# Kernel optimization log

Hardware: AMD Instinct MI355X
Metric: run time of the kernel (lower is better)

The kernel has to match this reference:

```python
import jax, jax.numpy as jnp
import numpy as np
from jax import lax

B, T, IDIM, HDIM = 128, 256, 64, 128
TS, KS, OC1, ANF = 64, 3, 100, 64
S1 = TS - 3 * (KS - 1)   # 58: three VALID ks=3 stride-1 convs
S = S1 * S1              # 3364
HN = 2 * HDIM            # 256 = h_dim * l_dim (l_dim=2)
F = S + HN               # 3620
HID = F // 2             # 1810


def _conv(x, w, b):
    y = lax.conv_general_dilated(x, w, (1, 1), 'VALID',
                                 dimension_numbers=('NCHW', 'OIHW', 'NCHW'))
    return y + b[None, :, None, None]


def _lstm_layer(x, w_ih, w_hh, b_ih, b_hh):
    # x: [B, T, D] -> (outputs [B, T, H], final hidden [B, H]); PyTorch gate order i,f,g,o
    Bn = x.shape[0]
    h0 = jnp.zeros((Bn, HDIM), x.dtype)
    c0 = jnp.zeros((Bn, HDIM), x.dtype)
    def step(carry, xt):
        h, c = carry
        g = xt @ w_ih.T + h @ w_hh.T + b_ih + b_hh
        i, f, gg, o = jnp.split(g, 4, axis=-1)
        c = jax.nn.sigmoid(f) * c + jax.nn.sigmoid(i) * jnp.tanh(gg)
        h = jax.nn.sigmoid(o) * jnp.tanh(c)
        return (h, c), h
    (hT, cT), ys = lax.scan(step, (h0, c0), jnp.swapaxes(x, 0, 1))
    return jnp.swapaxes(ys, 0, 1), hT


def setup_inputs() -> dict:
    key = jax.random.key(0)
    k = jax.random.split(key, 30)
    s = 0.05
    H4 = 4 * HDIM
    return {
        'x1': jax.random.normal(k[0], (B, 3, TS, TS), jnp.float32),
        'x2': jax.random.normal(k[1], (B, T, IDIM), jnp.float32),
        # conv2a/conv2b: two Monte-Carlo weight samples of the same Bayesian conv2 layer
        'conv1_w': jax.random.normal(k[2], (OC1, 3, KS, KS), jnp.float32) * s,
        'conv1_b': jax.random.normal(k[3], (OC1,), jnp.float32) * s,
        'conv2a_w': jax.random.normal(k[4], (OC1, OC1, KS, KS), jnp.float32) * s,
        'conv2a_b': jax.random.normal(k[5], (OC1,), jnp.float32) * s,
        'conv2b_w': jax.random.normal(k[6], (OC1, OC1, KS, KS), jnp.float32) * s,
        'conv2b_b': jax.random.normal(k[7], (OC1,), jnp.float32) * s,
        'w_ih0': jax.random.normal(k[8], (H4, IDIM), jnp.float32) * s,
        'w_hh0': jax.random.normal(k[9], (H4, HDIM), jnp.float32) * s,
        'b_ih0': jax.random.normal(k[10], (H4,), jnp.float32) * s,
        'b_hh0': jax.random.normal(k[11], (H4,), jnp.float32) * s,
        'w_ih1': jax.random.normal(k[12], (H4, HDIM), jnp.float32) * s,
        'w_hh1': jax.random.normal(k[13], (H4, HDIM), jnp.float32) * s,
        'b_ih1': jax.random.normal(k[14], (H4,), jnp.float32) * s,
        'b_hh1': jax.random.normal(k[15], (H4,), jnp.float32) * s,
        'attn1_w': jax.random.normal(k[16], (ANF, F), jnp.float32) * s,
        'attn1_b': jax.random.normal(k[17], (ANF,), jnp.float32) * s,
        'attn2_w': jax.random.normal(k[18], (1, ANF), jnp.float32) * s,
        'attn2_b': jax.random.normal(k[19], (1,), jnp.float32) * s,
        'fc1_w': jax.random.normal(k[20], (HID, F), jnp.float32) * s,
        'fc1_b': jax.random.normal(k[21], (HID,), jnp.float32) * s,
        'fc2_w': jax.random.normal(k[22], (1, HID), jnp.float32) * s,
        'fc2_b': jax.random.normal(k[23], (1,), jnp.float32) * s,
    }


def reference(x1, x2, conv1_w, conv1_b, conv2a_w, conv2a_b, conv2b_w, conv2b_b,
              w_ih0, w_hh0, b_ih0, b_hh0, w_ih1, w_hh1, b_ih1, b_hh1,
              attn1_w, attn1_b, attn2_w, attn2_b, fc1_w, fc1_b, fc2_w, fc2_b):
    Bn = x1.shape[0]
    # CNN branch
    x = jax.nn.relu(_conv(x1, conv1_w, conv1_b))
    x = jax.nn.relu(_conv(x, conv2a_w, conv2a_b))
    x = jax.nn.relu(_conv(x, conv2b_w, conv2b_b))
    xd = x.reshape(Bn, OC1, S)                               # [B, oc1, S]
    # LSTM branch (2 layers, dropout in eval mode = identity)
    y0, h0f = _lstm_layer(x2, w_ih0, w_hh0, b_ih0, b_hh0)
    _, h1f = _lstm_layer(y0, w_ih1, w_hh1, b_ih1, b_hh1)
    hn = jnp.concatenate([h0f, h1f], axis=1)                 # [B, 2*h_dim]
    # Broadcast hidden state across channels (replaces the torch concat loop)
    hn_b = jnp.broadcast_to(hn[:, None, :], (Bn, OC1, HN))
    fused = jnp.concatenate([xd, hn_b], axis=2)              # [B, oc1, F]
    # Attention
    a = jnp.tanh(fused @ attn1_w.T + attn1_b)                # [B, oc1, anf]
    a = a @ attn2_w.T + attn2_b                              # [B, oc1, 1]
    a = jax.nn.softmax(a, axis=1)
    ctx = jnp.einsum('bcs,bco->bso', xd, a).reshape(Bn, S)   # [B, S]
    # Fusion MLP (dropout eval-mode identity)
    m = jnp.concatenate([ctx, hn], axis=1)                   # [B, F]
    h = jax.nn.relu(m @ fc1_w.T + fc1_b)
    return h @ fc2_w.T + fc2_b                               # [B, 1]
```

## Files before the change

### kernel.cpp

```cpp
#include <hip/hip_runtime.h>
#include <hip/hip_bf16.h>
#include <math.h>

#define BB 128
#define TT 256
#define IDIM 64
#define HD 128
#define G4 512
#define OC 100
#define W1 62
#define W2 60
#define W3 58
#define NPX1 (W1*W1)
#define NPX2 (W2*W2)
#define NPX3 (W3*W3)
#define SS NPX3
#define FF (SS + 2*HD)
#define HIDN 1810
#define ANF 64

typedef __hip_bfloat16 bf16;
typedef _Float16 f16;
typedef __attribute__((ext_vector_type(8))) short bf16x8;
typedef __attribute__((ext_vector_type(4))) short bf16x4;
typedef __attribute__((ext_vector_type(2))) _Float16 half2v;
typedef __attribute__((ext_vector_type(4))) float f32x4;

__device__ __forceinline__ float ldf(const float* p) { return *p; }
__device__ __forceinline__ float ldf(const bf16* p)  { return __bfloat162float(*p); }
__device__ __forceinline__ void  stf(float* p, float v) { *p = v; }
__device__ __forceinline__ void  stf(bf16* p, float v)  { *p = __float2bfloat16(v); }

__device__ __forceinline__ short f2bs(float v) {
    bf16 t = __float2bfloat16(v); short s; __builtin_memcpy(&s, &t, 2); return s;
}
__device__ __forceinline__ float fsig(float x) {
    return __builtin_amdgcn_rcpf(1.f + __expf(-x));
}
__device__ __forceinline__ float ftanh(float x) {
    float t = __expf(-2.f * fabsf(x));
    float r = __builtin_amdgcn_rcpf(1.f + t);
    float m = 1.f - 2.f * t * r;
    return copysignf(m, x);
}
__device__ __forceinline__ float fmix2(unsigned w, unsigned h, float acc) {
    half2v wv, hv;
    __builtin_memcpy(&wv, &w, 4);
    __builtin_memcpy(&hv, &h, 4);
    acc = fmaf((float)wv[0], (float)hv[0], acc);
    acc = fmaf((float)wv[1], (float)hv[1], acc);
    return acc;
}

__device__ __forceinline__ bf16x8 load8(const bf16* p) { return *(const bf16x8*)p; }
__device__ __forceinline__ bf16x8 load8(const float* p) {
    float4 x = *(const float4*)p;
    float4 y = *(const float4*)(p + 4);
    bf16x8 r;
    r[0] = f2bs(x.x); r[1] = f2bs(x.y); r[2] = f2bs(x.z); r[3] = f2bs(x.w);
    r[4] = f2bs(y.x); r[5] = f2bs(y.y); r[6] = f2bs(y.z); r[7] = f2bs(y.w);
    return r;
}

__global__ void zero_kernel(float* o, int n)
{
    int i = blockIdx.x * 256 + threadIdx.x;
    if (i < n) o[i] = 0.f;
}

__global__ __launch_bounds__(256)
void cvt4_bf16(const float* __restrict__ s, bf16* __restrict__ d, int n4)
{
    int i = blockIdx.x * 256 + threadIdx.x;
    if (i >= n4) return;
    float4 v = ((const float4*)s)[i];
    bf16x4 o;
    o[0] = f2bs(v.x); o[1] = f2bs(v.y); o[2] = f2bs(v.z); o[3] = f2bs(v.w);
    *(bf16x4*)(d + 4 * (size_t)i) = o;
}

__global__ __launch_bounds__(256)
void cvt4_f16(const float* __restrict__ s, f16* __restrict__ d, int n4)
{
    int i = blockIdx.x * 256 + threadIdx.x;
    if (i >= n4) return;
    float4 v = ((const float4*)s)[i];
    f16 o[4] = {(f16)v.x, (f16)v.y, (f16)v.z, (f16)v.w};
    *(uint2*)(d + 4 * (size_t)i) = *(uint2*)o;
}

__global__ __launch_bounds__(256)
void conv1_kernel(const float* __restrict__ x1,
                  const float* __restrict__ w,
                  const float* __restrict__ bias,
                  bf16* __restrict__ out)
{
    __shared__ float wl[2700];
    __shared__ float bl[OC];
    int tid = threadIdx.x;
    for (int i = tid; i < 2700; i += 256) wl[i] = w[i];
    if (tid < OC) bl[tid] = bias[tid];
    __syncthreads();
    int b  = blockIdx.x;
    int px = blockIdx.y * 256 + tid;
    if (px >= NPX1) return;
    int y = px / W1, x = px % W1;
    float in[3][3][3];
    const float* xb = x1 + (size_t)b * 3 * 64 * 64;
#pragma unroll
    for (int ic = 0; ic < 3; ic++)
#pragma unroll
        for (int r = 0; r < 3; r++)
#pragma unroll
            for (int c = 0; c < 3; c++)
                in[ic][r][c] = xb[(ic * 64 + y + r) * 64 + x + c];
    bf16* ob = out + (size_t)b * OC * NPX1 + px;
    for (int oc = 0; oc < OC; ++oc) {
        float acc = bl[oc];
        const float* wp = &wl[oc * 27];
#pragma unroll
        for (int ic = 0; ic < 3; ic++)
#pragma unroll
            for (int r = 0; r < 3; r++)
#pragma unroll
                for (int c = 0; c < 3; c++)
                    acc = fmaf(in[ic][r][c], wp[ic * 9 + r * 3 + c], acc);
        ob[(size_t)oc * NPX1] = __float2bfloat16(fmaxf(acc, 0.f));
    }
}

__global__ __launch_bounds__(256)
void wt_repack(const float* __restrict__ w, bf16* __restrict__ WT)
{
    int idx = blockIdx.x * 256 + threadIdx.x;
    if (idx >= 129024) return;
    int i  = idx & 31;
    int oc = (idx >> 5) % 112;
    int ts = idx / (112 * 32);
    int s = ts & 3, t = ts >> 2;
    int ic = s * 32 + i;
    float v = 0.f;
    if (oc < OC && ic < OC) v = w[(oc * OC + ic) * 9 + t];
    WT[idx] = __float2bfloat16(v);
}

__global__ __launch_bounds__(512, 1)
void conv2_mfma(const bf16* __restrict__ in,
                const bf16* __restrict__ WT,
                const float* __restrict__ bias,
                bf16* __restrict__ out,
                int iw, int ow)
{
    __shared__ bf16 il[10 * 72 * 40];
    __shared__ bf16 wl[4032 * 8];
    int tid = threadIdx.x;
    int b = blockIdx.x;
    int y0 = blockIdx.y * 8;
    int wid = tid >> 6;
    int l = tid & 63;
    int hq = l >> 4;
    int l16 = l & 15;
    int yo = y0 + wid;

    f32x4 acc[7][4];
#pragma unroll
    for (int f = 0; f < 7; f++) {
#pragma unroll
        for (int r = 0; r < 4; r++) {
            int oc = f * 16 + hq * 4 + r;
            float bv = (oc < OC) ? bias[oc] : 0.f;
#pragma unroll
            for (int n = 0; n < 4; n++) acc[f][n][r] = bv;
        }
    }

    const size_t ims = (size_t)iw * iw;
    int icl = tid & 31;
    int t2  = tid >> 5;
    for (int s = 0; s < 4; ++s) {
        __syncthreads();
        int ic = s * 32 + icl;
        bool icok = ic < OC;
        const bf16* ibase = in + (size_t)(b * OC + ic) * ims;
#pragma unroll
        for (int it = 0; it < 6; ++it) {
            int u2 = t2 + it * 16;
            if (u2 < 90) {
                int r = u2 / 9, xb = u2 - r * 9;
                int x8 = xb * 8;
                int yy = y0 + r;
                bf16x8 v = {0, 0, 0, 0, 0, 0, 0, 0};
                if (icok && yy < iw && x8 < iw) {
                    const short* sp = (const short*)(ibase + (size_t)yy * iw + x8);
                    if (x8 + 8 <= iw) {
                        const unsigned* sp32 = (const unsigned*)sp;
#pragma unroll
                        for (int q = 0; q < 4; q++)
                            ((unsigned*)&v)[q] = sp32[q];
                    } else {
                        for (int k = 0; k < 8; k++)
                            if (x8 + k < iw) ((short*)&v)[k] = sp[k];
                    }
                }
                bf16* dst = &il[(r * 72 + x8) * 40 + icl];
#pragma unroll
                for (int k = 0; k < 8; k++)
                    *(short*)&dst[k * 40] = ((short*)&v)[k];
            }
        }
#pragma unroll
        for (int it = 0; it < 8; ++it) {
            int u = tid + it * 512;
            if (u < 4032) {
                int t = u / 448; int rem = u - t * 448;
                int oc = rem >> 2; int hq2 = rem & 3;
                *(bf16x8*)&wl[(size_t)((t * 4 + hq2) * 112 + oc) * 8] =
                    *(const bf16x8*)(WT + (size_t)((t * 4 + s) * 112 + oc) * 32 + hq2 * 8);
            }
        }
        __syncthreads();

#pragma unroll
        for (int ky = 0; ky < 3; ++ky) {
#pragma unroll
            for (int kx = 0; kx < 3; ++kx) {
                int t = ky * 3 + kx;
                bf16x8 a[7];
#pragma unroll
                for (int f = 0; f < 7; f++)
                    a[f] = *(const bf16x8*)&wl[(size_t)((t * 4 + hq) * 112 + f * 16 + l16) * 8];
                bf16x8 bfr[4];
#pragma unroll
                for (int n = 0; n < 4; n++)
                    bfr[n] = *(const bf16x8*)&il[((wid + ky) * 72 + kx + l16 + n * 16) * 40 + hq * 8];
#pragma unroll
                for (int f = 0; f < 7; f++)
#pragma unroll
                    for (int n = 0; n < 4; n++)
                        acc[f][n] = __builtin_amdgcn_mfma_f32_16x16x32_bf16(
                            a[f], bfr[n], acc[f][n], 0, 0, 0);
            }
        }
    }

    if (yo < ow) {
#pragma unroll
        for (int f = 0; f < 7; f++) {
#pragma unroll
            for (int r = 0; r < 4; r++) {
                int oc = f * 16 + hq * 4 + r;
                if (oc < OC) {
#pragma unroll
                    for (int n = 0; n < 4; n++) {
                        int x = n * 16 + l16;
                        if (x < ow)
                            out[((size_t)(b * OC + oc) * ow + yo) * ow + x] =
                                __float2bfloat16(fmaxf(acc[f][n][r], 0.f));
                    }
                }
            }
        }
    }
}

template<typename TB, typename TC, int ACT>
__global__ __launch_bounds__(256)
void gemm_mfma(const bf16* __restrict__ A, int lda,
               const TB* __restrict__ B, int ldb,
               const float* __restrict__ bias,
               TC* __restrict__ C, int ldc,
               int M, int N, int K)
{
    __shared__ bf16 As[64 * 72];
    __shared__ bf16 Bs[64 * 72];
    int tid = threadIdx.x;
    int l = tid & 63, wid = tid >> 6;
    int l16 = l & 15, h = l >> 4;
    int m0 = blockIdx.x * 64, n0 = blockIdx.y * 64;
    f32x4 acc[4];
#pragma unroll
    for (int nb = 0; nb < 4; nb++) acc[nb] = (f32x4){0.f, 0.f, 0.f, 0.f};

    int rs = tid >> 3;
    int kc = (tid & 7) * 8;

    for (int k0 = 0; k0 < K; k0 += 64) {
        int kr = K - k0;
#pragma unroll
        for (int half = 0; half < 2; half++) {
            int rr = rs + half * 32;
            bf16x8 av = {0, 0, 0, 0, 0, 0, 0, 0};
            int m = m0 + rr;
            if (m < M) {
                const short* src = (const short*)(A + (size_t)m * lda + k0 + kc);
                if (kc + 8 <= kr) av = *(const bf16x8*)src;
                else if (kc < kr) {
                    for (int j = 0; j < 8; j++) if (kc + j < kr) ((short*)&av)[j] = src[j];
                }
            }
            *(bf16x8*)&As[rr * 72 + kc] = av;
            bf16x8 bv = {0, 0, 0, 0, 0, 0, 0, 0};
            int n = n0 + rr;
            if (n < N) {
                const TB* src = B + (size_t)n * ldb + k0 + kc;
                if (kc + 8 <= kr) bv = load8(src);
                else if (kc < kr) {
                    for (int j = 0; j < 8; j++) if (kc + j < kr) ((short*)&bv)[j] = f2bs(ldf(src + j));
                }
            }
            *(bf16x8*)&Bs[rr * 72 + kc] = bv;
        }
        __syncthreads();
#pragma unroll
        for (int kk = 0; kk < 2; kk++) {
            bf16x8 af = *(const bf16x8*)&As[(wid * 16 + l16) * 72 + kk * 32 + h * 8];
#pragma unroll
            for (int nb = 0; nb < 4; nb++) {
                bf16x8 bfr = *(const bf16x8*)&Bs[(nb * 16 + l16) * 72 + kk * 32 + h * 8];
                acc[nb] = __builtin_amdgcn_mfma_f32_16x16x32_bf16(af, bfr, acc[nb], 0, 0, 0);
            }
        }
        __syncthreads();
    }
#pragma unroll
    for (int nb = 0; nb < 4; nb++) {
        int col = n0 + nb * 16 + l16;
        if (col >= N) continue;
        float bv = bias ? bias[col] : 0.f;
#pragma unroll
        for (int reg = 0; reg < 4; reg++) {
            int row = m0 + wid * 16 + h * 4 + reg;
            if (row < M) {
                float v = acc[nb][reg] + bv;
                if (ACT == 1) v = fmaxf(v, 0.f);
                stf(&C[(size_t)row * ldc + col], v);
            }
        }
    }
}

template<typename TA, typename TC, int BM, int BN, int BK, int TM, int TN, int ACT>
__global__ __launch_bounds__((BM / TM) * (BN / TN))
void gemm_tn(const TA* __restrict__ A, int lda,
             const float* __restrict__ Bmat, int ldb,
             const float* __restrict__ bias,
             TC* __restrict__ C, int ldc,
             int M, int N, int K)
{
    constexpr int TX = BN / TN;
    constexpr int TY = BM / TM;
    constexpr int NT = TX * TY;
    __shared__ float As[BK][BM + 1];
    __shared__ float Bs[BK][BN + 1];
    int tid = threadIdx.x;
    int tx = tid % TX, ty = tid / TX;
    int m0 = blockIdx.x * BM, n0 = blockIdx.y * BN;
    float acc[TM][TN] = {};
    for (int k0 = 0; k0 < K; k0 += BK) {
        for (int idx = tid; idx < BM * BK; idx += NT) {
            int i = idx / BK, j = idx % BK;
            int m = m0 + i, k = k0 + j;
            As[j][i] = (m < M && k < K) ? ldf(&A[(size_t)m * lda + k]) : 0.f;
        }
        for (int idx = tid; idx < BN * BK; idx += NT) {
            int i = idx / BK, j = idx % BK;
            int n = n0 + i, k = k0 + j;
            Bs[j][i] = (n < N && k < K) ? Bmat[(size_t)n * ldb + k] : 0.f;
        }
        __syncthreads();
#pragma unroll
        for (int k = 0; k < BK; ++k) {
            float av[TM], bv[TN];
#pragma unroll
            for (int i = 0; i < TM; i++) av[i] = As[k][ty * TM + i];
#pragma unroll
            for (int j = 0; j < TN; j++) bv[j] = Bs[k][tx * TN + j];
#pragma unroll
            for (int i = 0; i < TM; i++)
#pragma unroll
                for (int j = 0; j < TN; j++)
                    acc[i][j] += av[i] * bv[j];
        }
        __syncthreads();
    }
#pragma unroll
    for (int i = 0; i < TM; i++) {
        int m = m0 + ty * TM + i;
        if (m >= M) continue;
#pragma unroll
        for (int j = 0; j < TN; j++) {
            int n = n0 + tx * TN + j;
            if (n >= N) continue;
            float v = acc[i][j] + (bias ? bias[n] : 0.f);
            if (ACT == 1) v = fmaxf(v, 0.f);
            stf(&C[(size_t)m * ldc + n], v);
        }
    }
}

__global__ __launch_bounds__(512, 1)
void lstm_recur(const bf16* __restrict__ G,
                const f16* __restrict__ LWr,
                bf16* __restrict__ Y,
                float* __restrict__ HN,
                int hoff)
{
    __shared__ __align__(16) f16 hl[HD];
    __shared__ float ex[G4];
    int g = threadIdx.x;
    int b = blockIdx.x;
    uint4 wv[16];
    const uint4* wp = (const uint4*)(LWr + (size_t)g * HD);
#pragma unroll
    for (int q = 0; q < 16; q++) wv[q] = wp[q];
#pragma unroll
    for (int q = 0; q < 16; q++)
        asm volatile("" : "+v"(wv[q].x), "+v"(wv[q].y), "+v"(wv[q].z), "+v"(wv[q].w));
    float c = 0.f;
    if (g < HD) hl[g] = (f16)0.f;
    __syncthreads();
    const bf16* Gb = G + (size_t)b * TT * G4 + g;
    for (int t = 0; t < TT; ++t) {
        float dot = __bfloat162float(Gb[(size_t)t * G4]);
        float a0 = 0.f, a1 = 0.f, a2 = 0.f, a3 = 0.f;
#pragma unroll
        for (int q = 0; q < 16; q++) {
            uint4 hw = *(const uint4*)&hl[q * 8];
            a0 = fmix2(wv[q].x, hw.x, a0);
            a1 = fmix2(wv[q].y, hw.y, a1);
            a2 = fmix2(wv[q].z, hw.z, a2);
            a3 = fmix2(wv[q].w, hw.w, a3);
        }
        dot += (a0 + a1) + (a2 + a3);
        float tr;
        if (g < 2 * HD || g >= 3 * HD) tr = fsig(dot);
        else tr = ftanh(dot);
        ex[g] = tr;
        __syncthreads();
        if (g < HD) {
            float iv = ex[g], fv = ex[HD + g], gv = ex[2 * HD + g], ov = ex[3 * HD + g];
            c = fv * c + iv * gv;
            float nh = ov * ftanh(c);
            hl[g] = (f16)nh;
            if (Y) Y[((size_t)b * TT + t) * HD + g] = __float2bfloat16(nh);
            if (t == TT - 1) HN[(size_t)b * 256 + hoff + g] = nh;
        }
        __syncthreads();
    }
}

__global__ void bias_sum(const float* a, const float* b, float* o, int n)
{
    int i = blockIdx.x * 256 + threadIdx.x;
    if (i < n) o[i] = a[i] + b[i];
}

__global__ __launch_bounds__(128)
void attn_softmax(const float* __restrict__ T1,
                  const float* __restrict__ HB,
                  const float* __restrict__ a2w,
                  const float* __restrict__ a2b,
                  float* __restrict__ ATT)
{
    __shared__ float hbl[ANF];
    __shared__ float awl[ANF];
    __shared__ float red[128];
    int b = blockIdx.x, tid = threadIdx.x;
    if (tid < ANF) { hbl[tid] = HB[b * ANF + tid]; awl[tid] = a2w[tid]; }
    __syncthreads();
    float lg = -1e30f;
    if (tid < OC) {
        const float* tp = T1 + (size_t)(b * OC + tid) * ANF;
        float s = 0.f;
#pragma unroll 4
        for (int j = 0; j < ANF; j++) s += ftanh(tp[j] + hbl[j]) * awl[j];
        lg = s + a2b[0];
    }
    red[tid] = lg; __syncthreads();
    for (int st = 64; st > 0; st >>= 1) { if (tid < st) red[tid] = fmaxf(red[tid], red[tid + st]); __syncthreads(); }
    float mx = red[0]; __syncthreads();
    float e = (tid < OC) ? __expf(lg - mx) : 0.f;
    red[tid] = e; __syncthreads();
    for (int st = 64; st > 0; st >>= 1) { if (tid < st) red[tid] += red[tid + st]; __syncthreads(); }
    if (tid < OC) ATT[b * OC + tid] = e / red[0];
}

__global__ __launch_bounds__(256)
void ctx_concat(const bf16* __restrict__ XD,
                const float* __restrict__ ATT,
                const float* __restrict__ HN,
                bf16* __restrict__ M)
{
    __shared__ float al[OC];
    int b = blockIdx.x;
    int tid = threadIdx.x;
    if (tid < OC) al[tid] = ATT[b * OC + tid];
    __syncthreads();
    int s = blockIdx.y * 256 + tid;
    if (s < SS) {
        const bf16* xp = XD + (size_t)b * OC * SS + s;
        float acc = 0.f;
#pragma unroll 4
        for (int c = 0; c < OC; c++) acc = fmaf(__bfloat162float(xp[(size_t)c * SS]), al[c], acc);
        M[(size_t)b * FF + s] = __float2bfloat16(acc);
    } else if (s < FF) {
        M[(size_t)b * FF + s] = __float2bfloat16(HN[b * 256 + (s - SS)]);
    }
}

__global__ __launch_bounds__(256)
void fc2_kernel(const float* __restrict__ H1,
                const float* __restrict__ w,
                const float* __restrict__ bias,
                float* __restrict__ out)
{
    int tid = threadIdx.x;
    int lane = tid & 63, wid = tid >> 6;
    int b = blockIdx.x * 4 + wid;
    float acc = 0.f;
    for (int j = lane; j < HIDN; j += 64) acc = fmaf(H1[(size_t)b * HIDN + j], w[j], acc);
#pragma unroll
    for (int off = 32; off > 0; off >>= 1) acc += __shfl_down(acc, off, 64);
    if (lane == 0) out[b] = acc + bias[0];
}

extern "C" void kernel_launch(void* const* d_in, const int* in_sizes, int n_in,
                              void* d_out, int out_size, void* d_ws, size_t ws_size,
                              hipStream_t stream)
{
    const float* x1   = (const float*)d_in[0];
    const float* x2   = (const float*)d_in[1];
    const float* c1w  = (const float*)d_in[2];
    const float* c1b  = (const float*)d_in[3];
    const float* c2aw = (const float*)d_in[4];
    const float* c2ab = (const float*)d_in[5];
    const float* c2bw = (const float*)d_in[6];
    const float* c2bb = (const float*)d_in[7];
    const float* wih0 = (const float*)d_in[8];
    const float* whh0 = (const float*)d_in[9];
    const float* bih0 = (const float*)d_in[10];
    const float* bhh0 = (const float*)d_in[11];
    const float* wih1 = (const float*)d_in[12];
    const float* whh1 = (const float*)d_in[13];
    const float* bih1 = (const float*)d_in[14];
    const float* bhh1 = (const float*)d_in[15];
    const float* a1w  = (const float*)d_in[16];
    const float* a1b  = (const float*)d_in[17];
    const float* a2w  = (const float*)d_in[18];
    const float* a2b  = (const float*)d_in[19];
    const float* f1w  = (const float*)d_in[20];
    const float* f1b  = (const float*)d_in[21];
    const float* f2w  = (const float*)d_in[22];
    const float* f2b  = (const float*)d_in[23];
    float* out = (float*)d_out;

    char* base = (char*)d_ws;
    bf16* G0    = (bf16*)(base + 0);
    bf16* Y0    = (bf16*)(base + 33554432);
    bf16* G1    = G0;
    bf16* X2B   = (bf16*)(base + 41943040);
    bf16* WIH0B = (bf16*)(base + 46137344);
    bf16* WIH1B = (bf16*)(base + 46202880);
    f16*  LWf0  = (f16*)(base + 46333952);
    f16*  LWf1  = (f16*)(base + 46465024);
    const size_t LSTM_END = 46596096;

    int nb = 0; size_t ov = 0;
    for (int cand = BB; cand >= 32; cand >>= 1) {
        size_t cnn = (size_t)cand * OC * (NPX1 + NPX2) * 2;
        size_t o = cnn > LSTM_END ? cnn : LSTM_END;
        size_t q = o + 2048 + 2048 + 131072 + 32768
                 + (size_t)cand * OC * 64 * 4
                 + (((size_t)cand * OC * 4 + 255) & ~(size_t)255)
                 + 926720 + 926720 + 258048 + 258048 + 463360;
        if (ws_size >= q) { nb = cand; ov = o; break; }
    }
    if (nb == 0) {
        zero_kernel<<<1, 128, 0, stream>>>(out, out_size);
        return;
    }
    bf16* A1c = (bf16*)(base + 0);
    bf16* A2c = (bf16*)(base + (size_t)nb * OC * NPX1 * 2);
    bf16* XDc = A1c;
    size_t p = ov;
    float* BS0  = (float*)(base + p); p += 2048;
    float* BS1  = (float*)(base + p); p += 2048;
    float* HN   = (float*)(base + p); p += 131072;
    float* HB   = (float*)(base + p); p += 32768;
    float* T1c  = (float*)(base + p); p += (size_t)nb * OC * 64 * 4;
    float* ATTc = (float*)(base + p); p += ((size_t)nb * OC * 4 + 255) & ~(size_t)255;
    bf16*  MBb  = (bf16*)(base + p); p += 926720;
    float* H1   = (float*)(base + p); p += 926720;
    bf16* WTa   = (bf16*)(base + p); p += 258048;
    bf16* WTb   = (bf16*)(base + p); p += 258048;
    bf16* A1WB  = (bf16*)(base + p); p += 463360;

    wt_repack<<<504, 256, 0, stream>>>(c2aw, WTa);
    wt_repack<<<504, 256, 0, stream>>>(c2bw, WTb);
    cvt4_f16<<<64,   256, 0, stream>>>(whh0, LWf0, 16384);
    cvt4_f16<<<64,   256, 0, stream>>>(whh1, LWf1, 16384);
    cvt4_bf16<<<2048, 256, 0, stream>>>(x2,   X2B,   524288);
    cvt4_bf16<<<32,   256, 0, stream>>>(wih0, WIH0B, 8192);
    cvt4_bf16<<<64,   256, 0, stream>>>(wih1, WIH1B, 16384);
    cvt4_bf16<<<227,  256, 0, stream>>>(a1w,  A1WB,  57920);
    bias_sum<<<2, 256, 0, stream>>>(bih0, bhh0, BS0, G4);
    bias_sum<<<2, 256, 0, stream>>>(bih1, bhh1, BS1, G4);

    gemm_mfma<bf16, bf16, 0><<<dim3(512, 8), 256, 0, stream>>>(
        X2B, IDIM, WIH0B, IDIM, BS0, G0, G4, BB * TT, G4, IDIM);
    lstm_recur<<<BB, 512, 0, stream>>>(G0, LWf0, Y0, HN, 0);
    gemm_mfma<bf16, bf16, 0><<<dim3(512, 8), 256, 0, stream>>>(
        Y0, HD, WIH1B, HD, BS1, G1, G4, BB * TT, G4, HD);
    lstm_recur<<<BB, 512, 0, stream>>>(G1, LWf1, (bf16*)nullptr, HN, HD);

    gemm_tn<float, float, 32, 32, 16, 2, 2, 0><<<dim3(4, 2), 256, 0, stream>>>(
        HN, 256, a1w + SS, FF, a1b, HB, ANF, BB, ANF, 256);

    for (int c0 = 0; c0 < BB; c0 += nb) {
        conv1_kernel<<<dim3(nb, 16), 256, 0, stream>>>(
            x1 + (size_t)c0 * 3 * 64 * 64, c1w, c1b, A1c);
        conv2_mfma<<<dim3(nb, 8), 512, 0, stream>>>(A1c, WTa, c2ab, A2c, W1, W2);
        conv2_mfma<<<dim3(nb, 8), 512, 0, stream>>>(A2c, WTb, c2bb, XDc, W2, W3);
        gemm_mfma<bf16, float, 0><<<dim3(nb * OC / 64, 1), 256, 0, stream>>>(
            XDc, SS, A1WB, FF, nullptr, T1c, ANF, nb * OC, ANF, SS);
        attn_softmax<<<nb, 128, 0, stream>>>(T1c, HB + (size_t)c0 * ANF, a2w, a2b, ATTc);
        ctx_concat<<<dim3(nb, 15), 256, 0, stream>>>(
            XDc, ATTc, HN + (size_t)c0 * 256, MBb + (size_t)c0 * FF);
    }

    gemm_mfma<float, float, 1><<<dim3(2, 29), 256, 0, stream>>>(
        MBb, FF, f1w, FF, f1b, H1, HIDN, BB, HIDN, FF);
    fc2_kernel<<<BB / 4, 256, 0, stream>>>(H1, f2w, f2b, out);
}
```

Baseline: 1.229 ms.

## Merge preprocessing launches, relayout conv2 weight LDS, prefetch LSTM gate inputs

Ten small conversion, bias-sum and weight-repack launches are merged into one block-indexed prep kernel to cut launch overhead. The conv2 weight tile in LDS is stored so each lane's 16-byte A-fragment read is contiguous per wavefront, which should reduce bank conflicts. The LSTM recurrence now loads the next timestep's precomputed gate input before the current step's dot product, hiding global load latency behind the serial loop. These are three unrelated changes, and the merged prep kernel runs as a single grid with branch dispatch.

```diff
diff --git a/kernel.cpp b/kernel.cpp
--- a/kernel.cpp
+++ b/kernel.cpp
@@ -68,25 +68,60 @@
     if (i < n) o[i] = 0.f;
 }
 
-__global__ __launch_bounds__(256)
-void cvt4_bf16(const float* __restrict__ s, bf16* __restrict__ d, int n4)
-{
-    int i = blockIdx.x * 256 + threadIdx.x;
+__device__ __forceinline__ void body_cvt_bf16(const float* __restrict__ s, bf16* __restrict__ d,
+                                              int i, int n4)
+{
     if (i >= n4) return;
     float4 v = ((const float4*)s)[i];
     bf16x4 o;
     o[0] = f2bs(v.x); o[1] = f2bs(v.y); o[2] = f2bs(v.z); o[3] = f2bs(v.w);
     *(bf16x4*)(d + 4 * (size_t)i) = o;
 }
-
-__global__ __launch_bounds__(256)
-void cvt4_f16(const float* __restrict__ s, f16* __restrict__ d, int n4)
-{
-    int i = blockIdx.x * 256 + threadIdx.x;
+__device__ __forceinline__ void body_cvt_f16(const float* __restrict__ s, f16* __restrict__ d,
+                                             int i, int n4)
+{
     if (i >= n4) return;
     float4 v = ((const float4*)s)[i];
     f16 o[4] = {(f16)v.x, (f16)v.y, (f16)v.z, (f16)v.w};
     *(uint2*)(d + 4 * (size_t)i) = *(uint2*)o;
+}
+__device__ __forceinline__ void body_wt(const float* __restrict__ w, bf16* __restrict__ WT, int idx)
+{
+    if (idx >= 129024) return;
+    int i  = idx & 31;
+    int oc = (idx >> 5) % 112;
+    int ts = idx / (112 * 32);
+    int s = ts & 3, t = ts >> 2;
+    int ic = s * 32 + i;
+    float v = 0.f;
+    if (oc < OC && ic < OC) v = w[(oc * OC + ic) * 9 + t];
+    WT[idx] = __float2bfloat16(v);
+}
+
+__global__ __launch_bounds__(256)
+void prep_kernel(const float* __restrict__ x2,   bf16* __restrict__ X2B,
+                 const float* __restrict__ whh0, f16*  __restrict__ LWf0,
+                 const float* __restrict__ whh1, f16*  __restrict__ LWf1,
+                 const float* __restrict__ wih0, bf16* __restrict__ WIH0B,
+                 const float* __restrict__ wih1, bf16* __restrict__ WIH1B,
+                 const float* __restrict__ a1w,  bf16* __restrict__ A1WB,
+                 const float* __restrict__ bih0, const float* __restrict__ bhh0, float* __restrict__ BS0,
+                 const float* __restrict__ bih1, const float* __restrict__ bhh1, float* __restrict__ BS1,
+                 const float* __restrict__ c2aw, bf16* __restrict__ WTa,
+                 const float* __restrict__ c2bw, bf16* __restrict__ WTb)
+{
+    int bid = blockIdx.x;
+    int tid = threadIdx.x;
+    if (bid < 2048)      body_cvt_bf16(x2,   X2B,   bid * 256 + tid, 524288);
+    else if (bid < 2112) body_cvt_f16 (whh0, LWf0, (bid - 2048) * 256 + tid, 16384);
+    else if (bid < 2176) body_cvt_f16 (whh1, LWf1, (bid - 2112) * 256 + tid, 16384);
+    else if (bid < 2208) body_cvt_bf16(wih0, WIH0B, (bid - 2176) * 256 + tid, 8192);
+    else if (bid < 2272) body_cvt_bf16(wih1, WIH1B, (bid - 2208) * 256 + tid, 16384);
+    else if (bid < 2499) body_cvt_bf16(a1w,  A1WB,  (bid - 2272) * 256 + tid, 57920);
+    else if (bid < 2500) { BS0[tid] = bih0[tid] + bhh0[tid]; BS0[tid + 256] = bih0[tid + 256] + bhh0[tid + 256]; }
+    else if (bid < 2501) { BS1[tid] = bih1[tid] + bhh1[tid]; BS1[tid + 256] = bih1[tid + 256] + bhh1[tid + 256]; }
+    else if (bid < 3005) body_wt(c2aw, WTa, (bid - 2501) * 256 + tid);
+    else                 body_wt(c2bw, WTb, (bid - 3005) * 256 + tid);
 }
 
 __global__ __launch_bounds__(256)
@@ -129,21 +164,6 @@
     }
 }
 
-__global__ __launch_bounds__(256)
-void wt_repack(const float* __restrict__ w, bf16* __restrict__ WT)
-{
-    int idx = blockIdx.x * 256 + threadIdx.x;
-    if (idx >= 129024) return;
-    int i  = idx & 31;
-    int oc = (idx >> 5) % 112;
-    int ts = idx / (112 * 32);
-    int s = ts & 3, t = ts >> 2;
-    int ic = s * 32 + i;
-    float v = 0.f;
-    if (oc < OC && ic < OC) v = w[(oc * OC + ic) * 9 + t];
-    WT[idx] = __float2bfloat16(v);
-}
-
 __global__ __launch_bounds__(512, 1)
 void conv2_mfma(const bf16* __restrict__ in,
                 const bf16* __restrict__ WT,
@@ -212,9 +232,11 @@
         for (int it = 0; it < 8; ++it) {
             int u = tid + it * 512;
             if (u < 4032) {
-                int t = u / 448; int rem = u - t * 448;
-                int oc = rem >> 2; int hq2 = rem & 3;
-                *(bf16x8*)&wl[(size_t)((t * 4 + hq2) * 112 + oc) * 8] =
+                int tf = u >> 6; int lp = u & 63;
+                int t = tf / 7, f = tf - t * 7;
+                int oc = f * 16 + (lp & 15);
+                int hq2 = lp >> 4;
+                *(bf16x8*)&wl[(size_t)u * 8] =
                     *(const bf16x8*)(WT + (size_t)((t * 4 + s) * 112 + oc) * 32 + hq2 * 8);
             }
         }
@@ -228,7 +250,7 @@
                 bf16x8 a[7];
 #pragma unroll
                 for (int f = 0; f < 7; f++)
-                    a[f] = *(const bf16x8*)&wl[(size_t)((t * 4 + hq) * 112 + f * 16 + l16) * 8];
+                    a[f] = *(const bf16x8*)&wl[(size_t)((t * 7 + f) * 64 + l) * 8];
                 bf16x8 bfr[4];
 #pragma unroll
                 for (int n = 0; n < 4; n++)
@@ -420,8 +442,10 @@
     if (g < HD) hl[g] = (f16)0.f;
     __syncthreads();
     const bf16* Gb = G + (size_t)b * TT * G4 + g;
+    float gcur = __bfloat162float(Gb[0]);
     for (int t = 0; t < TT; ++t) {
-        float dot = __bfloat162float(Gb[(size_t)t * G4]);
+        int tn = (t + 1 < TT) ? t + 1 : t;
+        bf16 gnext = Gb[(size_t)tn * G4];
         float a0 = 0.f, a1 = 0.f, a2 = 0.f, a3 = 0.f;
 #pragma unroll
         for (int q = 0; q < 16; q++) {
@@ -431,11 +455,12 @@
             a2 = fmix2(wv[q].z, hw.z, a2);
             a3 = fmix2(wv[q].w, hw.w, a3);
         }
-        dot += (a0 + a1) + (a2 + a3);
+        float dot = gcur + (a0 + a1) + (a2 + a3);
         float tr;
         if (g < 2 * HD || g >= 3 * HD) tr = fsig(dot);
         else tr = ftanh(dot);
         ex[g] = tr;
+        gcur = __bfloat162float(gnext);
         __syncthreads();
         if (g < HD) {
             float iv = ex[g], fv = ex[HD + g], gv = ex[2 * HD + g], ov = ex[3 * HD + g];
@@ -447,12 +472,6 @@
         }
         __syncthreads();
     }
-}
-
-__global__ void bias_sum(const float* a, const float* b, float* o, int n)
-{
-    int i = blockIdx.x * 256 + threadIdx.x;
-    if (i < n) o[i] = a[i] + b[i];
 }
 
 __global__ __launch_bounds__(128)
@@ -595,16 +614,9 @@
     bf16* WTb   = (bf16*)(base + p); p += 258048;
     bf16* A1WB  = (bf16*)(base + p); p += 463360;
 
-    wt_repack<<<504, 256, 0, stream>>>(c2aw, WTa);
-    wt_repack<<<504, 256, 0, stream>>>(c2bw, WTb);
-    cvt4_f16<<<64,   256, 0, stream>>>(whh0, LWf0, 16384);
-    cvt4_f16<<<64,   256, 0, stream>>>(whh1, LWf1, 16384);
-    cvt4_bf16<<<2048, 256, 0, stream>>>(x2,   X2B,   524288);
-    cvt4_bf16<<<32,   256, 0, stream>>>(wih0, WIH0B, 8192);
-    cvt4_bf16<<<64,   256, 0, stream>>>(wih1, WIH1B, 16384);
-    cvt4_bf16<<<227,  256, 0, stream>>>(a1w,  A1WB,  57920);
-    bias_sum<<<2, 256, 0, stream>>>(bih0, bhh0, BS0, G4);
-    bias_sum<<<2, 256, 0, stream>>>(bih1, bhh1, BS1, G4);
+    prep_kernel<<<3509, 256, 0, stream>>>(
+        x2, X2B, whh0, LWf0, whh1, LWf1, wih0, WIH0B, wih1, WIH1B, a1w, A1WB,
+        bih0, bhh0, BS0, bih1, bhh1, BS1, c2aw, WTa, c2bw, WTb);
 
     gemm_mfma<bf16, bf16, 0><<<dim3(512, 8), 256, 0, stream>>>(
         X2B, IDIM, WIH0B, IDIM, BS0, G0, G4, BB * TT, G4, IDIM);
```

New measurement: 1.192 ms. -3.0%, faster.
